# Kernel tuning notes

Measured on AMD Instinct MI355X. Metric: run time of the kernel, lower is better.

The kernel has to match this reference:

```python
import jax, jax.numpy as jnp
import numpy as np

N = 20000      # nodes
E = 320000     # edges (avg degree 16)
DIN = 50       # PPI input features
C = 121        # PPI classes
HID = 1024     # 4 heads x 256 concatenated
H3 = 6         # heads in last layer


def setup_inputs() -> dict:
    key = jax.random.key(0)
    ks = jax.random.split(key, 7)
    X = jax.random.normal(ks[0], (N, DIN), jnp.float32)
    edge_index = jax.random.randint(ks[1], (2, E), 0, N, dtype=jnp.int32)
    def w(k, i, o):
        return jax.random.normal(k, (i, o), jnp.float32) / jnp.sqrt(jnp.float32(i))
    return {
        "X": X,
        "edge_index": edge_index,
        "W1": w(ks[2], DIN, HID),        # 4 heads x 256, concatenated
        "W2": w(ks[3], HID, HID),        # 4 heads x 256 GCN weights
        "S2": w(ks[4], HID, HID),        # 4 heads x 256 skip linears
        "W3": w(ks[5], HID, H3 * C),     # 6 heads x num_classes GCN weights
        "S3": w(ks[6], HID, H3 * C),     # 6 heads x num_classes skip linears
    }


def _agg(xw, row, col, norm, n):
    # GCN symmetric-normalized neighbor sum: out[col] += norm * xw[row]
    return jax.ops.segment_sum(xw[row] * norm[:, None], col, num_segments=n)


def reference(X, edge_index, W1, W2, S2, W3, S3):
    n = X.shape[0]
    row, col = edge_index[0], edge_index[1]
    # degree at targets (add_self_loops=False), D^{-1/2} A D^{-1/2} normalization
    deg = jax.ops.segment_sum(jnp.ones(row.shape, X.dtype), col, num_segments=n)
    dis = jnp.where(deg > 0, deg ** -0.5, 0.0)
    norm = dis[row] * dis[col]
    # layer 1: 4 GCN heads (weights concatenated), elu, concat
    h1 = jax.nn.elu(_agg(X @ W1, row, col, norm, n))              # [N, 1024]
    # layer 2: 4 GCN heads + linear skip, elu, concat
    h2 = jax.nn.elu(_agg(h1 @ W2, row, col, norm, n) + h1 @ S2)   # [N, 1024]
    # layer 3: 6 GCN heads + linear skip, average over heads (Identity act)
    y = _agg(h2 @ W3, row, col, norm, n) + h2 @ S3                # [N, 6*C]
    return y.reshape(n, H3, C).mean(axis=1)                       # [N, C]
```

## Files before the change

kernel.cpp:

```cpp
#include <hip/hip_runtime.h>
#include <hip/hip_bf16.h>
#include <math.h>

#define N_NODES 20000
#define N_EDGES 320000
#define DIN 50
#define HID 1024
#define NC3 726
#define NCLS 121
#define KCAT 2048
#define NQ 242

typedef __attribute__((ext_vector_type(8))) _Float16 half8;
typedef __attribute__((ext_vector_type(4))) float floatx4;

__device__ __forceinline__ unsigned short f2h(float v) {
    _Float16 h = (_Float16)v;
    return __builtin_bit_cast(unsigned short, h);
}
__device__ __forceinline__ float h2f(unsigned short u) {
    return (float)__builtin_bit_cast(_Float16, u);
}

__device__ __forceinline__ void async16(const void* g, void* l) {
    __builtin_amdgcn_global_load_lds(
        (const __attribute__((address_space(1))) void*)g,
        (__attribute__((address_space(3))) void*)l,
        16, 0, 0);
}


__global__ void zero_int_kernel(int* p, int n) {
    int i = blockIdx.x * blockDim.x + threadIdx.x;
    if (i < n) p[i] = 0;
}

__global__ void count_deg_kernel(const int* __restrict__ col, int* __restrict__ deg, int e) {
    int i = blockIdx.x * blockDim.x + threadIdx.x;
    if (i < e) atomicAdd(&deg[col[i]], 1);
}

__global__ __launch_bounds__(1024) void scan_kernel(const int* __restrict__ deg,
                                                    int* __restrict__ offs,
                                                    int* __restrict__ cursor,
                                                    float* __restrict__ dis,
                                                    int n, int total) {
    __shared__ int part[1024];
    int t = threadIdx.x;
    const int CH = (n + 1023) / 1024;
    int base0 = t * CH;
    int s = 0;
    for (int i = 0; i < CH; ++i) {
        int idx = base0 + i;
        if (idx < n) s += deg[idx];
    }
    part[t] = s;
    __syncthreads();
    for (int d = 1; d < 1024; d <<= 1) {
        int v = (t >= d) ? part[t - d] : 0;
        __syncthreads();
        part[t] += v;
        __syncthreads();
    }
    int run = part[t] - s;
    for (int i = 0; i < CH; ++i) {
        int idx = base0 + i;
        if (idx < n) {
            int d = deg[idx];
            offs[idx] = run;
            cursor[idx] = run;
            dis[idx] = d > 0 ? rsqrtf((float)d) : 0.0f;
            run += d;
        }
    }
    if (t == 1023) offs[n] = total;
}

__global__ void scatter_kernel(const int* __restrict__ row, const int* __restrict__ col,
                               const float* __restrict__ dis, int* __restrict__ cursor,
                               int* __restrict__ csr_src, float* __restrict__ csr_w, int e) {
    int i = blockIdx.x * blockDim.x + threadIdx.x;
    if (i < e) {
        int r = row[i], c = col[i];
        float nm = dis[r] * dis[c];
        int pos = atomicAdd(&cursor[c], 1);
        csr_src[pos] = r;
        csr_w[pos] = nm;
    }
}


__global__ void w1t_kernel(const float* __restrict__ W1, unsigned short* __restrict__ Bt1) {
    int i = blockIdx.x * blockDim.x + threadIdx.x;
    if (i >= HID * 64) return;
    int n = i / 64, k = i - n * 64;
    Bt1[i] = (k < DIN) ? f2h(W1[(size_t)k * HID + n]) : (unsigned short)0;
}

__global__ __launch_bounds__(256) void wt2_transpose_kernel(const float* __restrict__ W2,
                                                            const float* __restrict__ S2,
                                                            unsigned short* __restrict__ Th) {
    __shared__ unsigned short tile[32][33];
    int tb = blockIdx.x;
    int src = tb >> 10;
    int t = tb & 1023;
    int k0 = (t >> 5) * 32;
    int n0 = (t & 31) * 32;
    const float* W = src ? S2 : W2;
    int koff = src ? HID : 0;
    int tx = threadIdx.x & 31;
    int ty = threadIdx.x >> 5;
#pragma unroll
    for (int r = 0; r < 32; r += 8)
        tile[ty + r][tx] = f2h(W[(size_t)(k0 + ty + r) * HID + n0 + tx]);
    __syncthreads();
#pragma unroll
    for (int r = 0; r < 32; r += 8)
        Th[(size_t)(n0 + ty + r) * KCAT + koff + k0 + tx] = tile[tx][ty + r];
}

__global__ void foldsum_kernel(const float* __restrict__ W3, const float* __restrict__ S3,
                               float* __restrict__ T) {
    int i = blockIdx.x * blockDim.x + threadIdx.x;
    if (i >= 2 * HID * 128) return;
    int src = i >> 17;
    int r = i & 131071;
    int k = r >> 7, c = r & 127;
    const float* W = src ? S3 : W3;
    float v = 0.0f;
    if (c < NCLS) {
        const float* p = W + (size_t)k * NC3 + c;
        v = (p[0] + p[121] + p[242] + p[363] + p[484] + p[605]) * (1.0f / 6.0f);
    }
    T[(size_t)src * 131072 + r] = v;
}

__global__ __launch_bounds__(256) void wt3_transpose_kernel(const float* __restrict__ T,
                                                            unsigned short* __restrict__ Th) {
    __shared__ unsigned short tile[32][33];
    int tb = blockIdx.x;
    int src = tb >> 7;
    int t = tb & 127;
    int k0 = (t >> 2) * 32;
    int c0 = (t & 3) * 32;
    int tx = threadIdx.x & 31;
    int ty = threadIdx.x >> 5;
    const float* Tp = T + (size_t)src * 131072;
#pragma unroll
    for (int r = 0; r < 32; r += 8)
        tile[ty + r][tx] = f2h(Tp[(size_t)(k0 + ty + r) * 128 + c0 + tx]);
    __syncthreads();
#pragma unroll
    for (int r = 0; r < 32; r += 8) {
        int c = c0 + ty + r;
        if (c < NCLS)
            Th[(size_t)(src * NCLS + c) * HID + k0 + tx] = tile[tx][ty + r];
    }
}


__global__ __launch_bounds__(64) void aggX_kernel(const float* __restrict__ X,
                                                  const int* __restrict__ offs,
                                                  const int* __restrict__ csr_src,
                                                  const float* __restrict__ csr_w,
                                                  unsigned short* __restrict__ gX) {
    int n = blockIdx.x;
    int t = threadIdx.x;
    float a = 0.0f;
    if (t < DIN) {
        int p0 = offs[n], p1 = offs[n + 1];
        for (int p = p0; p < p1; ++p) {
            a = fmaf(csr_w[p], X[(size_t)csr_src[p] * DIN + t], a);
        }
    }
    gX[(size_t)n * 64 + t] = (t < DIN) ? f2h(a) : (unsigned short)0;
}

__global__ __launch_bounds__(256) void agg_slice_kernel(const unsigned short* __restrict__ h,
                                                        const int* __restrict__ offs,
                                                        const int* __restrict__ csr_src,
                                                        const float* __restrict__ csr_w,
                                                        unsigned short* __restrict__ g) {
    const int f = blockIdx.x;
    const int slice = f & 7;
    const int nb = f >> 3;
    const int tid = threadIdx.x;
    const int n = nb * 16 + (tid >> 4);
    const int coloff = slice * 128 + (tid & 15) * 8;
    const unsigned short* hp = h + coloff;

    float a[8] = {0, 0, 0, 0, 0, 0, 0, 0};
    int p0 = offs[n], p1 = offs[n + 1];
    for (int p = p0; p < p1; ++p) {
        int s = csr_src[p];
        float w = csr_w[p];
        uint4 v = *(const uint4*)&hp[(size_t)s * HID];
        const unsigned short* vs = (const unsigned short*)&v;
#pragma unroll
        for (int j = 0; j < 8; ++j) a[j] = fmaf(w, h2f(vs[j]), a[j]);
    }
    unsigned short ov[8];
#pragma unroll
    for (int j = 0; j < 8; ++j) ov[j] = f2h(a[j]);
    *(uint4*)&g[(size_t)n * HID + coloff] = *(const uint4*)ov;
}

__global__ __launch_bounds__(256) void agg3_kernel(const unsigned short* __restrict__ Q,
                                                   const int* __restrict__ offs,
                                                   const int* __restrict__ csr_src,
                                                   const float* __restrict__ csr_w,
                                                   float* __restrict__ out) {
    int n = blockIdx.x * 2 + (threadIdx.x >> 7);
    int c = threadIdx.x & 127;
    if (c >= NCLS) return;
    float a = 0.0f;
    int p0 = offs[n], p1 = offs[n + 1];
    for (int p = p0; p < p1; ++p) {
        a = fmaf(csr_w[p], h2f(Q[(size_t)csr_src[p] * NQ + c]), a);
    }
    a += h2f(Q[(size_t)n * NQ + NCLS + c]);
    out[(size_t)n * NCLS + c] = a;
}


#define GBM 128
#define GBN 128
#define GBK 32

template <int EPI>
__global__ __launch_bounds__(256, 4) void mfma_gemm_kernel(
        const unsigned short* __restrict__ Ag, const unsigned short* __restrict__ Ah,
        const unsigned short* __restrict__ Bt,
        void* __restrict__ Co,
        int M, int N, int ldc, int ktot, int khalf, int kw,
        int NB, int MB, int mchunk) {
    __shared__ __align__(16) unsigned short sA[2][GBM * GBK];
    __shared__ __align__(16) unsigned short sB[2][GBN * GBK];

    const int f = blockIdx.x;
    const int xcd = f & 7;
    const int r0 = f >> 3;
    const int nB = r0 % NB;
    const int mi = r0 / NB;
    const int mB = xcd * mchunk + mi;
    if (mB >= MB) return;
    const int bm = mB * GBM;
    const int bn = nB * GBN;
    const int ks = blockIdx.y;

    const int tid = threadIdx.x;
    const int lane = tid & 63;
    const int wave = tid >> 6;
    const int wm = wave >> 1;
    const int wn = wave & 1;

    const int st_r = tid >> 2;
    const int st_slot = tid & 3;
    const int st_c = (st_slot ^ ((st_r >> 1) & 3)) * 8;
    const int st_lds = st_r * GBK + st_slot * 8;

    int agm[2], bgn[2];
#pragma unroll
    for (int p = 0; p < 2; ++p) {
        int gm = bm + st_r + p * 64;
        agm[p] = gm < M ? gm : M - 1;
        int gn = bn + st_r + p * 64;
        bgn[p] = gn < N ? gn : N - 1;
    }

    const int frow = lane & 15;
    const int fkc = (((lane >> 4) ^ ((frow >> 1) & 3))) * 8;

    floatx4 acc[4][4];
#pragma unroll
    for (int i = 0; i < 4; ++i)
#pragma unroll
        for (int j = 0; j < 4; ++j) acc[i][j] = (floatx4){0.f, 0.f, 0.f, 0.f};

    auto issue = [&](int k0, int buf) {
        const unsigned short* ap = (k0 < khalf) ? Ag : Ah;
        int ka = (k0 < khalf) ? k0 : k0 - khalf;
#pragma unroll
        for (int p = 0; p < 2; ++p) {
            async16(&ap[(size_t)agm[p] * khalf + ka + st_c],
                    &sA[buf][p * 64 * GBK + st_lds]);
            async16(&Bt[(size_t)bgn[p] * ktot + k0 + st_c],
                    &sB[buf][p * 64 * GBK + st_lds]);
        }
    };

    const int tw = kw / GBK;
    const int t0 = ks * tw;
    const int t1 = t0 + tw;

    issue(t0 * GBK, 0);

    for (int t = t0; t < t1; ++t) {
        __syncthreads();
        if (t + 1 < t1) issue((t + 1) * GBK, (t + 1) & 1);

        const unsigned short* a_base = sA[t & 1];
        const unsigned short* b_base = sB[t & 1];
        half8 fa[4], fb[4];
#pragma unroll
        for (int i = 0; i < 4; ++i)
            fa[i] = *(const half8*)&a_base[(wm * 64 + i * 16 + frow) * GBK + fkc];
#pragma unroll
        for (int j = 0; j < 4; ++j)
            fb[j] = *(const half8*)&b_base[(wn * 64 + j * 16 + frow) * GBK + fkc];
#pragma unroll
        for (int i = 0; i < 4; ++i)
#pragma unroll
            for (int j = 0; j < 4; ++j)
                acc[i][j] = __builtin_amdgcn_mfma_f32_16x16x32_f16(fa[i], fb[j], acc[i][j], 0, 0, 0);
    }

    const int c_r0 = (lane >> 4) * 4;
    const int c_c = lane & 15;
#pragma unroll
    for (int i = 0; i < 4; ++i)
#pragma unroll
        for (int j = 0; j < 4; ++j) {
            int gn = bn + wn * 64 + j * 16 + c_c;
            if (gn >= N) continue;
#pragma unroll
            for (int r = 0; r < 4; ++r) {
                int gm = bm + wm * 64 + i * 16 + c_r0 + r;
                if (gm >= M) continue;
                float v = acc[i][j][r];
                if (EPI == 0) {
                    v = v > 0 ? v : expf(v) - 1.0f;
                    ((unsigned short*)Co)[(size_t)gm * ldc + gn] = f2h(v);
                } else if (EPI == 1) {
                    atomicAdd(&((float*)Co)[(size_t)gm * ldc + gn], v);
                } else {
                    ((unsigned short*)Co)[(size_t)gm * ldc + gn] = f2h(v);
                }
            }
        }
}


static inline size_t align_up(size_t x, size_t a) { return (x + a - 1) & ~(a - 1); }

extern "C" void kernel_launch(void* const* d_in, const int* in_sizes, int n_in,
                              void* d_out, int out_size, void* d_ws, size_t ws_size,
                              hipStream_t stream) {
    const float* X  = (const float*)d_in[0];
    const int* erow = (const int*)d_in[1];
    const int* ecol = (const int*)d_in[1] + N_EDGES;
    const float* W1 = (const float*)d_in[2];
    const float* W2 = (const float*)d_in[3];
    const float* S2 = (const float*)d_in[4];
    const float* W3 = (const float*)d_in[5];
    const float* S3 = (const float*)d_in[6];
    float* out = (float*)d_out;

    char* w = (char*)d_ws;
    int* deg     = (int*)w;             w += align_up((size_t)N_NODES * 4, 256);
    int* offs    = (int*)w;             w += align_up((size_t)(N_NODES + 1) * 4, 256);
    int* cursor  = (int*)w;             w += align_up((size_t)N_NODES * 4, 256);
    int* csr_src = (int*)w;             w += align_up((size_t)N_EDGES * 4, 256);
    float* dis   = (float*)w;           w += align_up((size_t)N_NODES * 4, 256);
    float* csr_w = (float*)w;           w += align_up((size_t)N_EDGES * 4, 256);
    float* Tfold = (float*)w;           w += align_up((size_t)2 * HID * 128 * 4, 256);
    unsigned short* gXh = (unsigned short*)w; w += align_up((size_t)N_NODES * 64 * 2, 256);
    unsigned short* h1 = (unsigned short*)w;  w += align_up((size_t)N_NODES * HID * 2, 256);
    unsigned short* g  = (unsigned short*)w;  w += align_up((size_t)N_NODES * HID * 2, 256);
    unsigned short* h2 = (unsigned short*)w;  w += align_up((size_t)N_NODES * HID * 2, 256);
    unsigned short* Qh = (unsigned short*)w;  w += align_up((size_t)N_NODES * NQ * 2, 256);
    unsigned short* Bt1 = (unsigned short*)w; w += align_up((size_t)HID * 64 * 2, 256);
    unsigned short* Bt2 = (unsigned short*)w; w += align_up((size_t)HID * KCAT * 2, 256);
    unsigned short* Bt3 = (unsigned short*)w; w += align_up((size_t)NQ * HID * 2, 256);

    const int TB = 256;
    int nb_n = (N_NODES + TB - 1) / TB;
    int nb_e = (N_EDGES + TB - 1) / TB;

    zero_int_kernel<<<nb_n, TB, 0, stream>>>(deg, N_NODES);
    count_deg_kernel<<<nb_e, TB, 0, stream>>>(ecol, deg, N_EDGES);
    scan_kernel<<<1, 1024, 0, stream>>>(deg, offs, cursor, dis, N_NODES, N_EDGES);
    scatter_kernel<<<nb_e, TB, 0, stream>>>(erow, ecol, dis, cursor, csr_src, csr_w, N_EDGES);

    w1t_kernel<<<(HID * 64 + 255) / 256, 256, 0, stream>>>(W1, Bt1);
    wt2_transpose_kernel<<<2048, 256, 0, stream>>>(W2, S2, Bt2);
    foldsum_kernel<<<(2 * HID * 128 + 255) / 256, 256, 0, stream>>>(W3, S3, Tfold);
    wt3_transpose_kernel<<<256, 256, 0, stream>>>(Tfold, Bt3);

    const int MB = (N_NODES + GBM - 1) / GBM;
    const int mchunk = (MB + 7) / 8;
    const int NB2 = HID / GBN;
    const int NB3 = (NQ + GBN - 1) / GBN;
    const int AGG_GRID = 8 * (N_NODES / 16);

    aggX_kernel<<<N_NODES, 64, 0, stream>>>(X, offs, csr_src, csr_w, gXh);
    mfma_gemm_kernel<0><<<dim3(8 * mchunk * NB2, 1), 256, 0, stream>>>(
        gXh, gXh, Bt1, h1, N_NODES, HID, HID, 64, 64, 64, NB2, MB, mchunk);

    agg_slice_kernel<<<AGG_GRID, 256, 0, stream>>>(h1, offs, csr_src, csr_w, g);
    mfma_gemm_kernel<0><<<dim3(8 * mchunk * NB2, 1), 256, 0, stream>>>(
        g, h1, Bt2, h2, N_NODES, HID, HID, KCAT, HID, KCAT, NB2, MB, mchunk);

    mfma_gemm_kernel<2><<<dim3(8 * mchunk * NB3, 1), 256, 0, stream>>>(
        h2, h2, Bt3, Qh, N_NODES, NQ, NQ, HID, HID, HID, NB3, MB, mchunk);
    agg3_kernel<<<N_NODES / 2, 256, 0, stream>>>(Qh, offs, csr_src, csr_w, out);
}
```

Measured before the change: 495.7 us.

## Merge weight-prep and degree-count kernels into one launch; group GEMM tiles along M

Folds the degree count, W1 transpose, W2/S2 transpose and the W3/S3 head-fold plus transpose into a single prep kernel, dispatched by block index. This drops four launches and the intermediate Tfold buffer. The GEMM block-to-tile mapping now walks groups of four M tiles per N tile, aiming for better L2 reuse of the B operand. The fused prep kernel may mix divergent block types, and the remap changes the cache access pattern.

```diff
diff --git a/kernel.cpp b/kernel.cpp
--- a/kernel.cpp
+++ b/kernel.cpp
@@ -33,11 +33,6 @@
 __global__ void zero_int_kernel(int* p, int n) {
     int i = blockIdx.x * blockDim.x + threadIdx.x;
     if (i < n) p[i] = 0;
-}
-
-__global__ void count_deg_kernel(const int* __restrict__ col, int* __restrict__ deg, int e) {
-    int i = blockIdx.x * blockDim.x + threadIdx.x;
-    if (i < e) atomicAdd(&deg[col[i]], 1);
 }
 
 __global__ __launch_bounds__(1024) void scan_kernel(const int* __restrict__ deg,
@@ -89,72 +84,69 @@
     }
 }
 
-
-__global__ void w1t_kernel(const float* __restrict__ W1, unsigned short* __restrict__ Bt1) {
-    int i = blockIdx.x * blockDim.x + threadIdx.x;
-    if (i >= HID * 64) return;
-    int n = i / 64, k = i - n * 64;
-    Bt1[i] = (k < DIN) ? f2h(W1[(size_t)k * HID + n]) : (unsigned short)0;
-}
-
-__global__ __launch_bounds__(256) void wt2_transpose_kernel(const float* __restrict__ W2,
-                                                            const float* __restrict__ S2,
-                                                            unsigned short* __restrict__ Th) {
+__global__ __launch_bounds__(256) void prep_kernel(const int* __restrict__ ecol,
+                                                   int* __restrict__ deg,
+                                                   const float* __restrict__ W1,
+                                                   unsigned short* __restrict__ Bt1,
+                                                   const float* __restrict__ W2,
+                                                   const float* __restrict__ S2,
+                                                   unsigned short* __restrict__ Bt2,
+                                                   const float* __restrict__ W3,
+                                                   const float* __restrict__ S3,
+                                                   unsigned short* __restrict__ Bt3) {
     __shared__ unsigned short tile[32][33];
-    int tb = blockIdx.x;
-    int src = tb >> 10;
-    int t = tb & 1023;
-    int k0 = (t >> 5) * 32;
-    int n0 = (t & 31) * 32;
-    const float* W = src ? S2 : W2;
-    int koff = src ? HID : 0;
-    int tx = threadIdx.x & 31;
-    int ty = threadIdx.x >> 5;
-#pragma unroll
-    for (int r = 0; r < 32; r += 8)
-        tile[ty + r][tx] = f2h(W[(size_t)(k0 + ty + r) * HID + n0 + tx]);
-    __syncthreads();
-#pragma unroll
-    for (int r = 0; r < 32; r += 8)
-        Th[(size_t)(n0 + ty + r) * KCAT + koff + k0 + tx] = tile[tx][ty + r];
-}
-
-__global__ void foldsum_kernel(const float* __restrict__ W3, const float* __restrict__ S3,
-                               float* __restrict__ T) {
-    int i = blockIdx.x * blockDim.x + threadIdx.x;
-    if (i >= 2 * HID * 128) return;
-    int src = i >> 17;
-    int r = i & 131071;
-    int k = r >> 7, c = r & 127;
-    const float* W = src ? S3 : W3;
-    float v = 0.0f;
-    if (c < NCLS) {
-        const float* p = W + (size_t)k * NC3 + c;
-        v = (p[0] + p[121] + p[242] + p[363] + p[484] + p[605]) * (1.0f / 6.0f);
-    }
-    T[(size_t)src * 131072 + r] = v;
-}
-
-__global__ __launch_bounds__(256) void wt3_transpose_kernel(const float* __restrict__ T,
-                                                            unsigned short* __restrict__ Th) {
-    __shared__ unsigned short tile[32][33];
-    int tb = blockIdx.x;
-    int src = tb >> 7;
-    int t = tb & 127;
-    int k0 = (t >> 2) * 32;
-    int c0 = (t & 3) * 32;
-    int tx = threadIdx.x & 31;
-    int ty = threadIdx.x >> 5;
-    const float* Tp = T + (size_t)src * 131072;
-#pragma unroll
-    for (int r = 0; r < 32; r += 8)
-        tile[ty + r][tx] = f2h(Tp[(size_t)(k0 + ty + r) * 128 + c0 + tx]);
-    __syncthreads();
-#pragma unroll
-    for (int r = 0; r < 32; r += 8) {
-        int c = c0 + ty + r;
-        if (c < NCLS)
-            Th[(size_t)(src * NCLS + c) * HID + k0 + tx] = tile[tx][ty + r];
+    const int b = blockIdx.x;
+    const int tid = threadIdx.x;
+
+    if (b < 2048) {
+        int src = b >> 10;
+        int t = b & 1023;
+        int k0 = (t >> 5) * 32;
+        int n0 = (t & 31) * 32;
+        const float* W = src ? S2 : W2;
+        int koff = src ? HID : 0;
+        int tx = tid & 31;
+        int ty = tid >> 5;
+#pragma unroll
+        for (int r = 0; r < 32; r += 8)
+            tile[ty + r][tx] = f2h(W[(size_t)(k0 + ty + r) * HID + n0 + tx]);
+        __syncthreads();
+#pragma unroll
+        for (int r = 0; r < 32; r += 8)
+            Bt2[(size_t)(n0 + ty + r) * KCAT + koff + k0 + tx] = tile[tx][ty + r];
+    } else if (b < 2304) {
+        int tb = b - 2048;
+        int src = tb >> 7;
+        int t = tb & 127;
+        int k0 = (t >> 2) * 32;
+        int c0 = (t & 3) * 32;
+        const float* W = src ? S3 : W3;
+        int tx = tid & 31;
+        int ty = tid >> 5;
+#pragma unroll
+        for (int r = 0; r < 32; r += 8) {
+            int k = k0 + ty + r, c = c0 + tx;
+            float v = 0.0f;
+            if (c < NCLS) {
+                const float* p = W + (size_t)k * NC3 + c;
+                v = (p[0] + p[121] + p[242] + p[363] + p[484] + p[605]) * (1.0f / 6.0f);
+            }
+            tile[ty + r][tx] = f2h(v);
+        }
+        __syncthreads();
+#pragma unroll
+        for (int r = 0; r < 32; r += 8) {
+            int c = c0 + ty + r;
+            if (c < NCLS)
+                Bt3[(size_t)(src * NCLS + c) * HID + k0 + tx] = tile[tx][ty + r];
+        }
+    } else if (b < 2560) {
+        int i = (b - 2304) * 256 + tid;
+        int n = i / 64, k = i - n * 64;
+        Bt1[i] = (k < DIN) ? f2h(W1[(size_t)k * HID + n]) : (unsigned short)0;
+    } else {
+        int i = (b - 2560) * 256 + tid;
+        if (i < N_EDGES) atomicAdd(&deg[ecol[i]], 1);
     }
 }
 
@@ -226,6 +218,7 @@
 #define GBM 128
 #define GBN 128
 #define GBK 32
+#define MII 4
 
 template <int EPI>
 __global__ __launch_bounds__(256, 4) void mfma_gemm_kernel(
@@ -240,8 +233,10 @@
     const int f = blockIdx.x;
     const int xcd = f & 7;
     const int r0 = f >> 3;
-    const int nB = r0 % NB;
-    const int mi = r0 / NB;
+    const int grp = r0 / (NB * MII);
+    const int rem = r0 % (NB * MII);
+    const int nB = rem / MII;
+    const int mi = grp * MII + rem % MII;
     const int mB = xcd * mchunk + mi;
     if (mB >= MB) return;
     const int bm = mB * GBM;
@@ -363,7 +358,6 @@
     int* csr_src = (int*)w;             w += align_up((size_t)N_EDGES * 4, 256);
     float* dis   = (float*)w;           w += align_up((size_t)N_NODES * 4, 256);
     float* csr_w = (float*)w;           w += align_up((size_t)N_EDGES * 4, 256);
-    float* Tfold = (float*)w;           w += align_up((size_t)2 * HID * 128 * 4, 256);
     unsigned short* gXh = (unsigned short*)w; w += align_up((size_t)N_NODES * 64 * 2, 256);
     unsigned short* h1 = (unsigned short*)w;  w += align_up((size_t)N_NODES * HID * 2, 256);
     unsigned short* g  = (unsigned short*)w;  w += align_up((size_t)N_NODES * HID * 2, 256);
@@ -375,17 +369,13 @@
 
     const int TB = 256;
     int nb_n = (N_NODES + TB - 1) / TB;
-    int nb_e = (N_EDGES + TB - 1) / TB;
 
     zero_int_kernel<<<nb_n, TB, 0, stream>>>(deg, N_NODES);
-    count_deg_kernel<<<nb_e, TB, 0, stream>>>(ecol, deg, N_EDGES);
+    prep_kernel<<<3810, 256, 0, stream>>>(ecol, deg, W1, Bt1, W2, S2, Bt2, W3, S3, Bt3);
+
     scan_kernel<<<1, 1024, 0, stream>>>(deg, offs, cursor, dis, N_NODES, N_EDGES);
-    scatter_kernel<<<nb_e, TB, 0, stream>>>(erow, ecol, dis, cursor, csr_src, csr_w, N_EDGES);
-
-    w1t_kernel<<<(HID * 64 + 255) / 256, 256, 0, stream>>>(W1, Bt1);
-    wt2_transpose_kernel<<<2048, 256, 0, stream>>>(W2, S2, Bt2);
-    foldsum_kernel<<<(2 * HID * 128 + 255) / 256, 256, 0, stream>>>(W3, S3, Tfold);
-    wt3_transpose_kernel<<<256, 256, 0, stream>>>(Tfold, Bt3);
+    scatter_kernel<<<(N_EDGES + TB - 1) / TB, TB, 0, stream>>>(erow, ecol, dis, cursor,
+                                                               csr_src, csr_w, N_EDGES);
 
     const int MB = (N_NODES + GBM - 1) / GBM;
     const int mchunk = (MB + 7) / 8;
```

Measured after the change: 489.4 us. Within noise of the previous version (-1.3%).
